# Kernel optimization log

Measured on AMD Instinct MI355X. Metric: run time of the kernel, lower is better.

The kernel has to match this reference:

```python
import jax, jax.numpy as jnp
import numpy as np

BLOCK = 16  # NVFP4 block size (one fp8e4m3 scale per 16 elements)
FP4_LEVELS = jnp.array([0.0, 0.5, 1.0, 1.5, 2.0, 3.0, 4.0, 6.0], dtype=jnp.float32)  # e2m1 magnitudes
FP4_MIDS = jnp.array([0.25, 0.75, 1.25, 1.75, 2.5, 3.5, 5.0], dtype=jnp.float32)     # round-to-nearest midpoints
FP8_MIN = 2.0 ** -9   # smallest positive fp8e4m3 subnormal (guards div-by-zero after scale cast)
FP8_MAX = 448.0


def fp8_e4m3_round(x):
    """Emulate casting positive float32 values to fp8 e4m3 (3 mantissa bits)."""
    e = jnp.clip(jnp.floor(jnp.log2(jnp.maximum(x, 1e-30))), -6.0, 8.0)  # -6 = min normal exponent
    step = jnp.exp2(e - 3.0)
    return jnp.clip(jnp.round(x / step) * step, 0.0, FP8_MAX)


def fp4_e2m1_quant(x):
    """Round-to-nearest onto the signed fp4 e2m1 grid {0,±0.5,±1,±1.5,±2,±3,±4,±6}."""
    idx = jnp.sum(jnp.abs(x)[..., None] > FP4_MIDS, axis=-1)
    return jnp.sign(x) * FP4_LEVELS[idx]


def quantize_activations(x2):
    """x2: [M, K] -> (fp4 values [M, K//16, 16], fp8 block scales [M, K//16])."""
    M, K = x2.shape
    xb = x2.reshape(M, K // BLOCK, BLOCK)
    amax = jnp.max(jnp.abs(xb), axis=-1)                      # per-16-block absmax
    s = jnp.maximum(fp8_e4m3_round(jnp.maximum(amax / 6.0, 1e-12)), FP8_MIN)
    q = fp4_e2m1_quant(xb / s[..., None])
    return q, s


def setup_inputs() -> dict:
    key = jax.random.key(0)
    k1, k2, k3 = jax.random.split(key, 3)
    in_f, out_f, tokens = 4096, 16384, 4096
    x = jax.random.normal(k1, (1, tokens, in_f), dtype=jnp.float32)
    # Build NVFP4 weights: quantize a random bf16-like weight per 16-element block.
    w = jax.random.normal(k2, (out_f, in_f), dtype=jnp.float32) * 0.02
    wb = w.reshape(out_f, in_f // BLOCK, BLOCK)
    weight_scale = jnp.maximum(fp8_e4m3_round(jnp.maximum(jnp.max(jnp.abs(wb), axis=-1) / 6.0, 1e-12)), FP8_MIN)
    weight_q = fp4_e2m1_quant(wb / weight_scale[..., None]).reshape(out_f, in_f)
    bias = jax.random.normal(k3, (out_f,), dtype=jnp.float32) * 0.01
    return {"x": x, "weight_q": weight_q, "weight_scale": weight_scale, "bias": bias}


def reference(x, weight_q, weight_scale, bias):
    orig_shape = x.shape
    K = orig_shape[-1]
    x2 = x.reshape(-1, K)                                     # [M, K]
    qa, sa = quantize_activations(x2)                          # fp4 values + fp8 block scales
    x_deq = (qa * sa[..., None]).reshape(x2.shape)             # dequantized activations
    N = weight_q.shape[0]
    w_deq = (weight_q.reshape(N, K // BLOCK, BLOCK) * weight_scale[..., None]).reshape(N, K)
    out = x2.dtype.type(0) + x_deq @ w_deq.T + bias[None, :]   # scaled_mm equivalent + bias
    return out.reshape(*orig_shape[:-1], N)
```

## Files before the change

### kernel.cpp

```cpp
#include <hip/hip_runtime.h>
#include <hip/hip_bf16.h>
#include <stdint.h>

typedef __attribute__((ext_vector_type(4))) float  f32x4;
typedef __attribute__((ext_vector_type(8))) short  bf16x8;
typedef __attribute__((ext_vector_type(8))) unsigned short u16x8;

#define MFMA16(d, x, y) d = __builtin_amdgcn_mfma_f32_16x16x32_bf16(x, y, d, 0, 0, 0)

static __device__ inline unsigned short f2bf(float f) {
    union { float f; unsigned u; } a; a.f = f;
    unsigned u = a.u;
    unsigned lsb = (u >> 16) & 1u;
    u += 0x7fffu + lsb;
    return (unsigned short)(u >> 16);
}

static __device__ inline float fp8_e4m3_round(float x) {
    union { float f; unsigned u; } a; a.f = x;
    int e = (int)((a.u >> 23) & 255u) - 127;
    e = e < -6 ? -6 : (e > 8 ? 8 : e);
    union { unsigned u; float f; } stp, inv;
    stp.u = (unsigned)(e - 3 + 127) << 23;
    inv.u = (unsigned)(3 - e + 127) << 23;
    float r = rintf(x * inv.f) * stp.f;
    return fminf(r, 448.0f);
}

static __device__ inline float fp4_level(float a) {
    return a > 2.5f ? (a > 3.5f ? (a > 5.0f ? 6.0f : 4.0f) : 3.0f)
                    : (a > 1.25f ? (a > 1.75f ? 2.0f : 1.5f)
                                 : (a > 0.75f ? 1.0f : (a > 0.25f ? 0.5f : 0.0f)));
}

__global__ void quant_x_kernel(const float* __restrict__ x, unsigned short* __restrict__ xd, int nblk) {
    int i = blockIdx.x * blockDim.x + threadIdx.x;
    if (i >= nblk) return;
    const float4* p = (const float4*)(x + (size_t)i * 16);
    float4 v0 = p[0], v1 = p[1], v2 = p[2], v3 = p[3];
    float vals[16] = { v0.x,v0.y,v0.z,v0.w, v1.x,v1.y,v1.z,v1.w,
                       v2.x,v2.y,v2.z,v2.w, v3.x,v3.y,v3.z,v3.w };
    float amax = 0.0f;
#pragma unroll
    for (int j = 0; j < 16; ++j) amax = fmaxf(amax, fabsf(vals[j]));
    float s0 = fmaxf(amax / 6.0f, 1e-12f);
    float s  = fmaxf(fp8_e4m3_round(s0), 1.0f / 512.0f);
    u16x8 o0, o1;
#pragma unroll
    for (int j = 0; j < 16; ++j) {
        float v = vals[j] / s;
        float lev = fp4_level(fabsf(v));
        float q = copysignf(lev, v);
        unsigned short b = f2bf(q * s);
        if (j < 8) o0[j] = b; else o1[j - 8] = b;
    }
    u16x8* dst = (u16x8*)(xd + (size_t)i * 16);
    dst[0] = o0; dst[1] = o1;
}

__global__ void deq_w_kernel(const float* __restrict__ wq, const float* __restrict__ wsc,
                             unsigned short* __restrict__ wd, int nblk) {
    int i = blockIdx.x * blockDim.x + threadIdx.x;
    if (i >= nblk) return;
    float s = wsc[i];
    const float4* p = (const float4*)(wq + (size_t)i * 16);
    float4 v0 = p[0], v1 = p[1], v2 = p[2], v3 = p[3];
    float vals[16] = { v0.x,v0.y,v0.z,v0.w, v1.x,v1.y,v1.z,v1.w,
                       v2.x,v2.y,v2.z,v2.w, v3.x,v3.y,v3.z,v3.w };
    u16x8 o0, o1;
#pragma unroll
    for (int j = 0; j < 16; ++j) {
        unsigned short b = f2bf(vals[j] * s);
        if (j < 8) o0[j] = b; else o1[j - 8] = b;
    }
    u16x8* dst = (u16x8*)(wd + (size_t)i * 16);
    dst[0] = o0; dst[1] = o1;
}

static __device__ __forceinline__ void stage_half(const unsigned short* g0, const unsigned short* g1,
                                                  size_t koff, char* d0) {
    __builtin_amdgcn_global_load_lds((const __attribute__((address_space(1))) void*)(g0 + koff),
                                     (__attribute__((address_space(3))) void*)d0, 16, 0, 0);
    __builtin_amdgcn_global_load_lds((const __attribute__((address_space(1))) void*)(g1 + koff),
                                     (__attribute__((address_space(3))) void*)(d0 + 1024), 16, 0, 0);
}

__global__ __launch_bounds__(512, 2)
void gemm_kernel(const unsigned short* __restrict__ A, const unsigned short* __restrict__ Bw,
                 const float* __restrict__ bias, float* __restrict__ C,
                 int M, int N, int K) {
    extern __shared__ char lds[];
    const int tid  = threadIdx.x;
    const int lane = tid & 63;
    const int wid  = tid >> 6;
    const int wr   = wid >> 2;
    const int wc   = wid & 3;

    const int NXB = N >> 8, NYB = M >> 8;
    int bid = blockIdx.x;
    int bx, by;
    if (NXB == 64 && NYB == 16) {
        int xcd = bid & 7, c = bid >> 3;
        bx = xcd * 8 + (c & 7);
        by = c >> 3;
    } else { bx = bid % NXB; by = bid / NXB; }

    const int NT = K >> 6;

    int w0 = (lane & 15) * 64 + ((lane >> 4) << 4);
    const int lane_off = w0 ^ (((w0 >> 9) & 1) << 5);
    const int u   = (lane * 16) ^ (lane & 32);
    const int r_l = u >> 6;
    const int c_l = (u & 63) >> 1;

    const unsigned short* gA0 = A  + (size_t)(by * 256 + wid * 32 + r_l) * K + c_l;
    const unsigned short* gA1 = gA0 + (size_t)16 * K;
    const unsigned short* gB0 = Bw + (size_t)(bx * 256 + wid * 32 + r_l) * K + c_l;
    const unsigned short* gB1 = gB0 + (size_t)16 * K;
    char* ldsA_w = lds + wid * 2048 + lane * 16;
    char* ldsB_w = lds + 65536 + wid * 2048 + lane * 16;

    f32x4 acc[8][4];
#pragma unroll
    for (int m = 0; m < 8; ++m)
#pragma unroll
        for (int n = 0; n < 4; ++n)
#pragma unroll
            for (int j = 0; j < 4; ++j) acc[m][n][j] = 0.0f;

    stage_half(gA0, gA1, 0,   ldsA_w);
    stage_half(gB0, gB1, 0,   ldsB_w);
    stage_half(gA0, gA1, 32,  ldsA_w + 16384);
    stage_half(gB0, gB1, 32,  ldsB_w + 16384);
    stage_half(gA0, gA1, 64,  ldsA_w + 32768);
    stage_half(gB0, gB1, 64,  ldsB_w + 32768);
    stage_half(gA0, gA1, 96,  ldsA_w + 32768 + 16384);
    asm volatile("s_waitcnt vmcnt(6)" ::: "memory");
    __builtin_amdgcn_s_barrier();

    bf16x8 a[8], bq[4];

    for (int t = 0; t <= NT - 3; ++t) {
        const int b = t & 1;
        const char* pA = lds + b * 32768 + wr * 8192 + lane_off;
        const char* pB = lds + 65536 + b * 32768 + wc * 4096 + lane_off;
        char* dA2 = ldsA_w + b * 32768;
        char* dB1 = ldsB_w + ((t + 1) & 1) * 32768;
        char* dB2 = ldsB_w + b * 32768;
        const size_t k1off = (size_t)(t + 1) * 64;
        const size_t k2off = (size_t)(t + 2) * 64;

        asm volatile("s_waitcnt vmcnt(6)" ::: "memory");
#pragma unroll
        for (int mf = 0; mf < 8; ++mf) a[mf] = *(const bf16x8*)(pA + mf * 1024);
        bq[0] = *(const bf16x8*)(pB);
        bq[1] = *(const bf16x8*)(pB + 1024);
        stage_half(gB0, gB1, k1off + 32, dB1 + 16384);
        __builtin_amdgcn_s_barrier();
        asm volatile("s_waitcnt lgkmcnt(0)" ::: "memory");
        __builtin_amdgcn_s_setprio(1);
#pragma unroll
        for (int mf = 0; mf < 8; ++mf) { MFMA16(acc[mf][0], a[mf], bq[0]); MFMA16(acc[mf][1], a[mf], bq[1]); }
        __builtin_amdgcn_s_setprio(0);
        __builtin_amdgcn_s_barrier();

        bq[2] = *(const bf16x8*)(pB + 2048);
        bq[3] = *(const bf16x8*)(pB + 3072);
        stage_half(gA0, gA1, k2off, dA2);
        __builtin_amdgcn_s_barrier();
        asm volatile("s_waitcnt lgkmcnt(0)" ::: "memory");
        __builtin_amdgcn_s_setprio(1);
#pragma unroll
        for (int mf = 0; mf < 8; ++mf) { MFMA16(acc[mf][2], a[mf], bq[2]); MFMA16(acc[mf][3], a[mf], bq[3]); }
        __builtin_amdgcn_s_setprio(0);
        __builtin_amdgcn_s_barrier();

        asm volatile("s_waitcnt vmcnt(6)" ::: "memory");
#pragma unroll
        for (int mf = 0; mf < 8; ++mf) a[mf] = *(const bf16x8*)(pA + 16384 + mf * 1024);
        bq[0] = *(const bf16x8*)(pB + 16384);
        bq[1] = *(const bf16x8*)(pB + 16384 + 1024);
        stage_half(gB0, gB1, k2off, dB2);
        __builtin_amdgcn_s_barrier();
        asm volatile("s_waitcnt lgkmcnt(0)" ::: "memory");
        __builtin_amdgcn_s_setprio(1);
#pragma unroll
        for (int mf = 0; mf < 8; ++mf) { MFMA16(acc[mf][0], a[mf], bq[0]); MFMA16(acc[mf][1], a[mf], bq[1]); }
        __builtin_amdgcn_s_setprio(0);
        __builtin_amdgcn_s_barrier();

        bq[2] = *(const bf16x8*)(pB + 16384 + 2048);
        bq[3] = *(const bf16x8*)(pB + 16384 + 3072);
        stage_half(gA0, gA1, k2off + 32, dA2 + 16384);
        __builtin_amdgcn_s_barrier();
        asm volatile("s_waitcnt lgkmcnt(0)" ::: "memory");
        __builtin_amdgcn_s_setprio(1);
#pragma unroll
        for (int mf = 0; mf < 8; ++mf) { MFMA16(acc[mf][2], a[mf], bq[2]); MFMA16(acc[mf][3], a[mf], bq[3]); }
        __builtin_amdgcn_s_setprio(0);
        __builtin_amdgcn_s_barrier();
    }

    {
        char* dBl = ldsB_w + ((NT - 1) & 1) * 32768;
        stage_half(gB0, gB1, (size_t)(NT - 1) * 64 + 32, dBl + 16384);
    }
    asm volatile("s_waitcnt vmcnt(0)" ::: "memory");
    __builtin_amdgcn_s_barrier();

#pragma unroll 1
    for (int tt = NT - 2; tt < NT; ++tt) {
        const int b = tt & 1;
        const char* pA = lds + b * 32768 + wr * 8192 + lane_off;
        const char* pB = lds + 65536 + b * 32768 + wc * 4096 + lane_off;
#pragma unroll
        for (int s = 0; s < 2; ++s) {
            bf16x8 a2[8], b2[4];
#pragma unroll
            for (int mf = 0; mf < 8; ++mf) a2[mf] = *(const bf16x8*)(pA + s * 16384 + mf * 1024);
#pragma unroll
            for (int nf = 0; nf < 4; ++nf) b2[nf] = *(const bf16x8*)(pB + s * 16384 + nf * 1024);
#pragma unroll
            for (int mf = 0; mf < 8; ++mf)
#pragma unroll
                for (int nf = 0; nf < 4; ++nf) MFMA16(acc[mf][nf], a2[mf], b2[nf]);
        }
    }

    const int row0 = by * 256 + wr * 128;
    const int col0 = bx * 256 + wc * 64;
#pragma unroll
    for (int nf = 0; nf < 4; ++nf) {
        int col = col0 + nf * 16 + (lane & 15);
        float bv = bias[col];
#pragma unroll
        for (int mf = 0; mf < 8; ++mf) {
#pragma unroll
            for (int j = 0; j < 4; ++j) {
                int row = row0 + mf * 16 + ((lane >> 4) << 2) + j;
                C[(size_t)row * N + col] = acc[mf][nf][j] + bv;
            }
        }
    }
}

extern "C" void kernel_launch(void* const* d_in, const int* in_sizes, int n_in,
                              void* d_out, int out_size, void* d_ws, size_t ws_size,
                              hipStream_t stream) {
    const float* x    = (const float*)d_in[0];
    const float* wq   = (const float*)d_in[1];
    const float* wsc  = (const float*)d_in[2];
    const float* bias = (const float*)d_in[3];
    float* out = (float*)d_out;

    const long N = in_sizes[3];
    const long K = (long)in_sizes[1] / N;
    const long M = (long)in_sizes[0] / K;

    size_t need = ((size_t)(M * K) + (size_t)(N * K)) * sizeof(unsigned short);
    if (ws_size < need) return;

    unsigned short* xd = (unsigned short*)d_ws;
    unsigned short* wd = xd + (size_t)M * K;

    {
        int nblk = (int)(M * K / 16);
        quant_x_kernel<<<(nblk + 255) / 256, 256, 0, stream>>>(x, xd, nblk);
    }
    {
        int nblk = (int)(N * K / 16);
        deq_w_kernel<<<(nblk + 255) / 256, 256, 0, stream>>>(wq, wsc, wd, nblk);
    }
    {
        hipFuncSetAttribute((const void*)gemm_kernel,
                            hipFuncAttributeMaxDynamicSharedMemorySize, 131072);
        int nwg = (int)((M / 256) * (N / 256));
        gemm_kernel<<<dim3(nwg), dim3(512), 131072, stream>>>(xd, wd, bias, out,
                                                              (int)M, (int)N, (int)K);
    }
}
```

Before: 539.9 us.

## Restructure GEMM main loop into register double-buffered M-half quadrants

The main loop now splits each K-step into M-half by full-N MFMA blocks instead of N-half by full-M blocks. A and B fragments are preloaded into separate register sets so LDS reads for the next quadrant or K-step are issued before the current MFMAs. Partial lgkmcnt waits and sched_barriers are meant to overlap LDS latency with matrix math. The cost is higher VGPR pressure from the extra fragment buffers, and the global-to-LDS staging order is changed, which risks data races if the barrier placement is wrong.

```diff
diff --git a/kernel.cpp b/kernel.cpp
--- a/kernel.cpp
+++ b/kernel.cpp
@@ -138,65 +138,85 @@
     asm volatile("s_waitcnt vmcnt(6)" ::: "memory");
     __builtin_amdgcn_s_barrier();
 
-    bf16x8 a[8], bq[4];
+    bf16x8 aK0a[4], aK0b[4], aK1a[4], aK1b[4], bK0[4], bK1[4];
+
+    {
+        const char* pA = lds + wr * 8192 + lane_off;
+        const char* pB = lds + 65536 + wc * 4096 + lane_off;
+#pragma unroll
+        for (int i = 0; i < 4; ++i) aK0a[i] = *(const bf16x8*)(pA + i * 1024);
+#pragma unroll
+        for (int i = 0; i < 4; ++i) bK0[i]  = *(const bf16x8*)(pB + i * 1024);
+    }
 
     for (int t = 0; t <= NT - 3; ++t) {
-        const int b = t & 1;
-        const char* pA = lds + b * 32768 + wr * 8192 + lane_off;
-        const char* pB = lds + 65536 + b * 32768 + wc * 4096 + lane_off;
+        const int b  = t & 1;
+        const int b1 = (t + 1) & 1;
+        const char* pA  = lds + b * 32768 + wr * 8192 + lane_off;
+        const char* pB  = lds + 65536 + b * 32768 + wc * 4096 + lane_off;
+        const char* pA1 = lds + b1 * 32768 + wr * 8192 + lane_off;
+        const char* pB1 = lds + 65536 + b1 * 32768 + wc * 4096 + lane_off;
         char* dA2 = ldsA_w + b * 32768;
-        char* dB1 = ldsB_w + ((t + 1) & 1) * 32768;
+        char* dB1 = ldsB_w + b1 * 32768;
         char* dB2 = ldsB_w + b * 32768;
         const size_t k1off = (size_t)(t + 1) * 64;
         const size_t k2off = (size_t)(t + 2) * 64;
 
+#pragma unroll
+        for (int i = 0; i < 4; ++i) aK0b[i] = *(const bf16x8*)(pA + (4 + i) * 1024);
+        stage_half(gB0, gB1, k1off + 32, dB1 + 16384);
+        __builtin_amdgcn_s_barrier();
+        __builtin_amdgcn_s_setprio(1);
+#pragma unroll
+        for (int m = 0; m < 4; ++m)
+#pragma unroll
+            for (int n = 0; n < 4; ++n) MFMA16(acc[m][n], aK0a[m], bK0[n]);
+        __builtin_amdgcn_s_setprio(0);
+        __builtin_amdgcn_s_barrier();
+
         asm volatile("s_waitcnt vmcnt(6)" ::: "memory");
 #pragma unroll
-        for (int mf = 0; mf < 8; ++mf) a[mf] = *(const bf16x8*)(pA + mf * 1024);
-        bq[0] = *(const bf16x8*)(pB);
-        bq[1] = *(const bf16x8*)(pB + 1024);
-        stage_half(gB0, gB1, k1off + 32, dB1 + 16384);
-        __builtin_amdgcn_s_barrier();
-        asm volatile("s_waitcnt lgkmcnt(0)" ::: "memory");
+        for (int i = 0; i < 4; ++i) aK1a[i] = *(const bf16x8*)(pA + 16384 + i * 1024);
+#pragma unroll
+        for (int i = 0; i < 4; ++i) bK1[i]  = *(const bf16x8*)(pB + 16384 + i * 1024);
+        __builtin_amdgcn_s_barrier();
+        asm volatile("s_waitcnt lgkmcnt(8)" ::: "memory");
+        __builtin_amdgcn_sched_barrier(0);
+        stage_half(gA0, gA1, k2off, dA2);
         __builtin_amdgcn_s_setprio(1);
 #pragma unroll
-        for (int mf = 0; mf < 8; ++mf) { MFMA16(acc[mf][0], a[mf], bq[0]); MFMA16(acc[mf][1], a[mf], bq[1]); }
+        for (int m = 0; m < 4; ++m)
+#pragma unroll
+            for (int n = 0; n < 4; ++n) MFMA16(acc[4 + m][n], aK0b[m], bK0[n]);
         __builtin_amdgcn_s_setprio(0);
         __builtin_amdgcn_s_barrier();
 
-        bq[2] = *(const bf16x8*)(pB + 2048);
-        bq[3] = *(const bf16x8*)(pB + 3072);
-        stage_half(gA0, gA1, k2off, dA2);
-        __builtin_amdgcn_s_barrier();
-        asm volatile("s_waitcnt lgkmcnt(0)" ::: "memory");
+#pragma unroll
+        for (int i = 0; i < 4; ++i) aK1b[i] = *(const bf16x8*)(pA + 16384 + (4 + i) * 1024);
+        stage_half(gB0, gB1, k2off, dB2);
+        __builtin_amdgcn_s_barrier();
         __builtin_amdgcn_s_setprio(1);
 #pragma unroll
-        for (int mf = 0; mf < 8; ++mf) { MFMA16(acc[mf][2], a[mf], bq[2]); MFMA16(acc[mf][3], a[mf], bq[3]); }
+        for (int m = 0; m < 4; ++m)
+#pragma unroll
+            for (int n = 0; n < 4; ++n) MFMA16(acc[m][n], aK1a[m], bK1[n]);
         __builtin_amdgcn_s_setprio(0);
         __builtin_amdgcn_s_barrier();
 
         asm volatile("s_waitcnt vmcnt(6)" ::: "memory");
 #pragma unroll
-        for (int mf = 0; mf < 8; ++mf) a[mf] = *(const bf16x8*)(pA + 16384 + mf * 1024);
-        bq[0] = *(const bf16x8*)(pB + 16384);
-        bq[1] = *(const bf16x8*)(pB + 16384 + 1024);
-        stage_half(gB0, gB1, k2off, dB2);
-        __builtin_amdgcn_s_barrier();
-        asm volatile("s_waitcnt lgkmcnt(0)" ::: "memory");
+        for (int i = 0; i < 4; ++i) aK0a[i] = *(const bf16x8*)(pA1 + i * 1024);
+#pragma unroll
+        for (int i = 0; i < 4; ++i) bK0[i]  = *(const bf16x8*)(pB1 + i * 1024);
+        __builtin_amdgcn_s_barrier();
+        asm volatile("s_waitcnt lgkmcnt(8)" ::: "memory");
+        __builtin_amdgcn_sched_barrier(0);
+        stage_half(gA0, gA1, k2off + 32, dA2 + 16384);
         __builtin_amdgcn_s_setprio(1);
 #pragma unroll
-        for (int mf = 0; mf < 8; ++mf) { MFMA16(acc[mf][0], a[mf], bq[0]); MFMA16(acc[mf][1], a[mf], bq[1]); }
-        __builtin_amdgcn_s_setprio(0);
-        __builtin_amdgcn_s_barrier();
-
-        bq[2] = *(const bf16x8*)(pB + 16384 + 2048);
-        bq[3] = *(const bf16x8*)(pB + 16384 + 3072);
-        stage_half(gA0, gA1, k2off + 32, dA2 + 16384);
-        __builtin_amdgcn_s_barrier();
-        asm volatile("s_waitcnt lgkmcnt(0)" ::: "memory");
-        __builtin_amdgcn_s_setprio(1);
-#pragma unroll
-        for (int mf = 0; mf < 8; ++mf) { MFMA16(acc[mf][2], a[mf], bq[2]); MFMA16(acc[mf][3], a[mf], bq[3]); }
+        for (int m = 0; m < 4; ++m)
+#pragma unroll
+            for (int n = 0; n < 4; ++n) MFMA16(acc[4 + m][n], aK1b[m], bK1[n]);
         __builtin_amdgcn_s_setprio(0);
         __builtin_amdgcn_s_barrier();
     }
```

Measured after the change: 559.4 us. 3.6% more time.

## Load B fragments directly from global into registers, stage only A in LDS

Applied to the files above, without the earlier changes.

The GEMM no longer stages the weight (B) tile through LDS. Each wave loads its B fragments straight from global memory into registers, double-buffered across iterations, while A is still staged with global_load_lds. The main loop is unrolled by two with a macro body, and LDS use drops from 128KB to 64KB. This removes LDS traffic and bank pressure for B, but each B element is now fetched from global once per wave row instead of once per workgroup (duplicated across the two wr waves), and it adds register pressure.

```diff
diff --git a/kernel.cpp b/kernel.cpp
--- a/kernel.cpp
+++ b/kernel.cpp
@@ -85,6 +85,60 @@
                                      (__attribute__((address_space(3))) void*)(d0 + 1024), 16, 0, 0);
 }
 
+#define LOADB4(dst, koff) {                                             \
+    dst[0] = *(const bf16x8*)(gBr + (size_t)(koff));                    \
+    dst[1] = *(const bf16x8*)(gBr + bstride + (size_t)(koff));          \
+    dst[2] = *(const bf16x8*)(gBr + 2 * bstride + (size_t)(koff));      \
+    dst[3] = *(const bf16x8*)(gBr + 3 * bstride + (size_t)(koff)); }
+
+#define MFMA_HALF(AV, BV, n0) {                                         \
+    _Pragma("unroll")                                                   \
+    for (int mf = 0; mf < 8; ++mf) {                                    \
+        MFMA16(acc[mf][n0], AV[mf], BV[n0]);                            \
+        MFMA16(acc[mf][n0 + 1], AV[mf], BV[n0 + 1]);                    \
+    } }
+
+#define BODY(T, BUFC, BUFN, K0C, K1C, K0N) {                                      \
+    const size_t t64 = (size_t)(T) * 64;                                          \
+                                                                          \
+    LOADB4(K1C, t64 + 32);                                                        \
+    __builtin_amdgcn_s_barrier();                                                 \
+    asm volatile("s_waitcnt lgkmcnt(0)" ::: "memory");                            \
+    __builtin_amdgcn_s_setprio(1);                                                \
+    MFMA_HALF(a, K0C, 0);                                                         \
+    __builtin_amdgcn_s_setprio(0);                                                \
+    __builtin_amdgcn_s_barrier();                                                 \
+                                                                          \
+    stage_half(gA0, gA1, t64 + 128, ldsA_w + (BUFC) * 32768);                     \
+    { const char* pc = lds + (BUFC) * 32768 + wr * 8192 + lane_off + 16384;       \
+      _Pragma("unroll")                                                           \
+      for (int i = 0; i < 8; ++i) a2[i] = *(const bf16x8*)(pc + i * 1024); }      \
+    asm volatile("s_waitcnt vmcnt(12)" ::: "memory");                             \
+    __builtin_amdgcn_s_barrier();                                                 \
+    __builtin_amdgcn_s_setprio(1);                                                \
+    MFMA_HALF(a, K0C, 2);                                                         \
+    __builtin_amdgcn_s_setprio(0);                                                \
+    __builtin_amdgcn_s_barrier();                                                 \
+                                                                          \
+    LOADB4(K0N, t64 + 64);                                                        \
+    __builtin_amdgcn_s_barrier();                                                 \
+    asm volatile("s_waitcnt lgkmcnt(0)" ::: "memory");                            \
+    __builtin_amdgcn_s_setprio(1);                                                \
+    MFMA_HALF(a2, K1C, 0);                                                        \
+    __builtin_amdgcn_s_setprio(0);                                                \
+    __builtin_amdgcn_s_barrier();                                                 \
+                                                                          \
+    stage_half(gA0, gA1, t64 + 160, ldsA_w + (BUFC) * 32768 + 16384);             \
+    { const char* pn = lds + (BUFN) * 32768 + wr * 8192 + lane_off;               \
+      _Pragma("unroll")                                                           \
+      for (int i = 0; i < 8; ++i) a[i] = *(const bf16x8*)(pn + i * 1024); }       \
+    asm volatile("s_waitcnt vmcnt(12)" ::: "memory");                             \
+    __builtin_amdgcn_s_barrier();                                                 \
+    __builtin_amdgcn_s_setprio(1);                                                \
+    MFMA_HALF(a2, K1C, 2);                                                        \
+    __builtin_amdgcn_s_setprio(0);                                                \
+    __builtin_amdgcn_s_barrier(); }
+
 __global__ __launch_bounds__(512, 2)
 void gemm_kernel(const unsigned short* __restrict__ A, const unsigned short* __restrict__ Bw,
                  const float* __restrict__ bias, float* __restrict__ C,
@@ -113,12 +167,13 @@
     const int r_l = u >> 6;
     const int c_l = (u & 63) >> 1;
 
-    const unsigned short* gA0 = A  + (size_t)(by * 256 + wid * 32 + r_l) * K + c_l;
+    const unsigned short* gA0 = A + (size_t)(by * 256 + wid * 32 + r_l) * K + c_l;
     const unsigned short* gA1 = gA0 + (size_t)16 * K;
-    const unsigned short* gB0 = Bw + (size_t)(bx * 256 + wid * 32 + r_l) * K + c_l;
-    const unsigned short* gB1 = gB0 + (size_t)16 * K;
     char* ldsA_w = lds + wid * 2048 + lane * 16;
-    char* ldsB_w = lds + 65536 + wid * 2048 + lane * 16;
+
+    const size_t bstride = (size_t)16 * K;
+    const unsigned short* gBr = Bw + (size_t)(bx * 256 + wc * 64 + (lane & 15)) * K
+                                   + ((lane >> 4) << 3);
 
     f32x4 acc[8][4];
 #pragma unroll
@@ -128,104 +183,52 @@
 #pragma unroll
             for (int j = 0; j < 4; ++j) acc[m][n][j] = 0.0f;
 
+    bf16x8 a[8], a2[8];
+    bf16x8 b0x[4], b1x[4], b0y[4], b1y[4];
+
     stage_half(gA0, gA1, 0,   ldsA_w);
-    stage_half(gB0, gB1, 0,   ldsB_w);
     stage_half(gA0, gA1, 32,  ldsA_w + 16384);
-    stage_half(gB0, gB1, 32,  ldsB_w + 16384);
     stage_half(gA0, gA1, 64,  ldsA_w + 32768);
-    stage_half(gB0, gB1, 64,  ldsB_w + 32768);
     stage_half(gA0, gA1, 96,  ldsA_w + 32768 + 16384);
-    asm volatile("s_waitcnt vmcnt(6)" ::: "memory");
+    LOADB4(b0x, 0);
+    asm volatile("s_waitcnt vmcnt(8)" ::: "memory");
     __builtin_amdgcn_s_barrier();
-
-    bf16x8 a[8], bq[4];
-
-    for (int t = 0; t <= NT - 3; ++t) {
-        const int b = t & 1;
-        const char* pA = lds + b * 32768 + wr * 8192 + lane_off;
-        const char* pB = lds + 65536 + b * 32768 + wc * 4096 + lane_off;
-        char* dA2 = ldsA_w + b * 32768;
-        char* dB1 = ldsB_w + ((t + 1) & 1) * 32768;
-        char* dB2 = ldsB_w + b * 32768;
-        const size_t k1off = (size_t)(t + 1) * 64;
-        const size_t k2off = (size_t)(t + 2) * 64;
-
-        asm volatile("s_waitcnt vmcnt(6)" ::: "memory");
-#pragma unroll
-        for (int mf = 0; mf < 8; ++mf) a[mf] = *(const bf16x8*)(pA + mf * 1024);
-        bq[0] = *(const bf16x8*)(pB);
-        bq[1] = *(const bf16x8*)(pB + 1024);
-        stage_half(gB0, gB1, k1off + 32, dB1 + 16384);
-        __builtin_amdgcn_s_barrier();
-        asm volatile("s_waitcnt lgkmcnt(0)" ::: "memory");
-        __builtin_amdgcn_s_setprio(1);
-#pragma unroll
-        for (int mf = 0; mf < 8; ++mf) { MFMA16(acc[mf][0], a[mf], bq[0]); MFMA16(acc[mf][1], a[mf], bq[1]); }
-        __builtin_amdgcn_s_setprio(0);
-        __builtin_amdgcn_s_barrier();
-
-        bq[2] = *(const bf16x8*)(pB + 2048);
-        bq[3] = *(const bf16x8*)(pB + 3072);
-        stage_half(gA0, gA1, k2off, dA2);
-        __builtin_amdgcn_s_barrier();
-        asm volatile("s_waitcnt lgkmcnt(0)" ::: "memory");
-        __builtin_amdgcn_s_setprio(1);
-#pragma unroll
-        for (int mf = 0; mf < 8; ++mf) { MFMA16(acc[mf][2], a[mf], bq[2]); MFMA16(acc[mf][3], a[mf], bq[3]); }
-        __builtin_amdgcn_s_setprio(0);
-        __builtin_amdgcn_s_barrier();
-
-        asm volatile("s_waitcnt vmcnt(6)" ::: "memory");
-#pragma unroll
-        for (int mf = 0; mf < 8; ++mf) a[mf] = *(const bf16x8*)(pA + 16384 + mf * 1024);
-        bq[0] = *(const bf16x8*)(pB + 16384);
-        bq[1] = *(const bf16x8*)(pB + 16384 + 1024);
-        stage_half(gB0, gB1, k2off, dB2);
-        __builtin_amdgcn_s_barrier();
-        asm volatile("s_waitcnt lgkmcnt(0)" ::: "memory");
-        __builtin_amdgcn_s_setprio(1);
-#pragma unroll
-        for (int mf = 0; mf < 8; ++mf) { MFMA16(acc[mf][0], a[mf], bq[0]); MFMA16(acc[mf][1], a[mf], bq[1]); }
-        __builtin_amdgcn_s_setprio(0);
-        __builtin_amdgcn_s_barrier();
-
-        bq[2] = *(const bf16x8*)(pB + 16384 + 2048);
-        bq[3] = *(const bf16x8*)(pB + 16384 + 3072);
-        stage_half(gA0, gA1, k2off + 32, dA2 + 16384);
-        __builtin_amdgcn_s_barrier();
-        asm volatile("s_waitcnt lgkmcnt(0)" ::: "memory");
-        __builtin_amdgcn_s_setprio(1);
-#pragma unroll
-        for (int mf = 0; mf < 8; ++mf) { MFMA16(acc[mf][2], a[mf], bq[2]); MFMA16(acc[mf][3], a[mf], bq[3]); }
-        __builtin_amdgcn_s_setprio(0);
-        __builtin_amdgcn_s_barrier();
-    }
-
-    {
-        char* dBl = ldsB_w + ((NT - 1) & 1) * 32768;
-        stage_half(gB0, gB1, (size_t)(NT - 1) * 64 + 32, dBl + 16384);
-    }
+    {
+        const char* p0 = lds + wr * 8192 + lane_off;
+#pragma unroll
+        for (int i = 0; i < 8; ++i) a[i] = *(const bf16x8*)(p0 + i * 1024);
+    }
+
+    for (int t = 0; t <= NT - 4; t += 2) {
+        BODY(t,     0, 1, b0x, b1x, b0y);
+        BODY(t + 1, 1, 0, b0y, b1y, b0x);
+    }
+
+    LOADB4(b1x, (size_t)(NT - 2) * 64 + 32);
+    LOADB4(b0y, (size_t)(NT - 1) * 64);
+    LOADB4(b1y, (size_t)(NT - 1) * 64 + 32);
     asm volatile("s_waitcnt vmcnt(0)" ::: "memory");
     __builtin_amdgcn_s_barrier();
-
-#pragma unroll 1
-    for (int tt = NT - 2; tt < NT; ++tt) {
-        const int b = tt & 1;
-        const char* pA = lds + b * 32768 + wr * 8192 + lane_off;
-        const char* pB = lds + 65536 + b * 32768 + wc * 4096 + lane_off;
-#pragma unroll
-        for (int s = 0; s < 2; ++s) {
-            bf16x8 a2[8], b2[4];
-#pragma unroll
-            for (int mf = 0; mf < 8; ++mf) a2[mf] = *(const bf16x8*)(pA + s * 16384 + mf * 1024);
-#pragma unroll
-            for (int nf = 0; nf < 4; ++nf) b2[nf] = *(const bf16x8*)(pB + s * 16384 + nf * 1024);
-#pragma unroll
-            for (int mf = 0; mf < 8; ++mf)
-#pragma unroll
-                for (int nf = 0; nf < 4; ++nf) MFMA16(acc[mf][nf], a2[mf], b2[nf]);
-        }
-    }
+    asm volatile("s_waitcnt lgkmcnt(0)" ::: "memory");
+    MFMA_HALF(a, b0x, 0); MFMA_HALF(a, b0x, 2);
+    {
+        const char* pc = lds + wr * 8192 + lane_off + 16384;
+#pragma unroll
+        for (int i = 0; i < 8; ++i) a2[i] = *(const bf16x8*)(pc + i * 1024);
+    }
+    MFMA_HALF(a2, b1x, 0); MFMA_HALF(a2, b1x, 2);
+    {
+        const char* pn = lds + 32768 + wr * 8192 + lane_off;
+#pragma unroll
+        for (int i = 0; i < 8; ++i) a[i] = *(const bf16x8*)(pn + i * 1024);
+    }
+    MFMA_HALF(a, b0y, 0); MFMA_HALF(a, b0y, 2);
+    {
+        const char* pn2 = lds + 32768 + wr * 8192 + lane_off + 16384;
+#pragma unroll
+        for (int i = 0; i < 8; ++i) a2[i] = *(const bf16x8*)(pn2 + i * 1024);
+    }
+    MFMA_HALF(a2, b1y, 0); MFMA_HALF(a2, b1y, 2);
 
     const int row0 = by * 256 + wr * 128;
     const int col0 = bx * 256 + wc * 64;
@@ -273,9 +276,9 @@
     }
     {
         hipFuncSetAttribute((const void*)gemm_kernel,
-                            hipFuncAttributeMaxDynamicSharedMemorySize, 131072);
+                            hipFuncAttributeMaxDynamicSharedMemorySize, 65536);
         int nwg = (int)((M / 256) * (N / 256));
-        gemm_kernel<<<dim3(nwg), dim3(512), 131072, stream>>>(xd, wd, bias, out,
-                                                              (int)M, (int)N, (int)K);
-    }
-}
+        gemm_kernel<<<dim3(nwg), dim3(512), 65536, stream>>>(xd, wd, bias, out,
+                                                             (int)M, (int)N, (int)K);
+    }
+}
```

Measured after the change: 1.039 ms. 92.4% more time.

## Register double-buffer LDS fragments and overlap reads with full MFMA phases

Applied to the files above, without the earlier changes.

Restructures the GEMM main loop so that each phase holds two register sets of A/B fragments. The next half-tile is read from LDS while the 32 MFMAs of the current half run, with one barrier per phase instead of four. Global-to-LDS staging is reorganised so both A and B halves load together, and the prologue and epilogue are adjusted to match. The aim is to hide LDS read latency and barrier overhead, at the cost of higher register pressure and less margin on the LDS write-after-read ordering.

```diff
diff --git a/kernel.cpp b/kernel.cpp
--- a/kernel.cpp
+++ b/kernel.cpp
@@ -85,6 +85,40 @@
                                      (__attribute__((address_space(3))) void*)(d0 + 1024), 16, 0, 0);
 }
 
+#define MFMA_ALL(AV, BV) {                                              \
+    _Pragma("unroll")                                                   \
+    for (int mf = 0; mf < 8; ++mf) {                                    \
+        _Pragma("unroll")                                               \
+        for (int nf = 0; nf < 4; ++nf) MFMA16(acc[mf][nf], AV[mf], BV[nf]); } }
+
+#define READ12(AV, BV, OFF) {                                           \
+    const char* _pa = lds + (OFF) + wr * 8192 + lane_off;               \
+    const char* _pb = lds + 65536 + (OFF) + wc * 4096 + lane_off;       \
+    _Pragma("unroll")                                                   \
+    for (int i = 0; i < 8; ++i) AV[i] = *(const bf16x8*)(_pa + i * 1024); \
+    _Pragma("unroll")                                                   \
+    for (int i = 0; i < 4; ++i) BV[i] = *(const bf16x8*)(_pb + i * 1024); }
+
+#define PH1(T, B) {                                                     \
+    asm volatile("s_waitcnt vmcnt(4)" ::: "memory");                    \
+    __builtin_amdgcn_s_barrier();                                       \
+    __builtin_amdgcn_s_setprio(1);                                      \
+    READ12(a2, b2, (B) * 32768 + 16384);                                \
+    stage_half(gA0, gA1, (size_t)((T) + 1) * 64 + 32, ldsA_w + (1 - (B)) * 32768 + 16384); \
+    stage_half(gB0, gB1, (size_t)((T) + 1) * 64 + 32, ldsB_w + (1 - (B)) * 32768 + 16384); \
+    MFMA_ALL(a1, b1);                                                   \
+    __builtin_amdgcn_s_setprio(0); }
+
+#define PH2(T, B) {                                                     \
+    asm volatile("s_waitcnt vmcnt(4)" ::: "memory");                    \
+    __builtin_amdgcn_s_barrier();                                       \
+    __builtin_amdgcn_s_setprio(1);                                      \
+    READ12(a1, b1, (1 - (B)) * 32768);                                  \
+    stage_half(gA0, gA1, (size_t)((T) + 2) * 64, ldsA_w + (B) * 32768); \
+    stage_half(gB0, gB1, (size_t)((T) + 2) * 64, ldsB_w + (B) * 32768); \
+    MFMA_ALL(a2, b2);                                                   \
+    __builtin_amdgcn_s_setprio(0); }
+
 __global__ __launch_bounds__(512, 2)
 void gemm_kernel(const unsigned short* __restrict__ A, const unsigned short* __restrict__ Bw,
                  const float* __restrict__ bias, float* __restrict__ C,
@@ -128,103 +162,36 @@
 #pragma unroll
             for (int j = 0; j < 4; ++j) acc[m][n][j] = 0.0f;
 
-    stage_half(gA0, gA1, 0,   ldsA_w);
-    stage_half(gB0, gB1, 0,   ldsB_w);
-    stage_half(gA0, gA1, 32,  ldsA_w + 16384);
-    stage_half(gB0, gB1, 32,  ldsB_w + 16384);
-    stage_half(gA0, gA1, 64,  ldsA_w + 32768);
-    stage_half(gB0, gB1, 64,  ldsB_w + 32768);
-    stage_half(gA0, gA1, 96,  ldsA_w + 32768 + 16384);
-    asm volatile("s_waitcnt vmcnt(6)" ::: "memory");
+    bf16x8 a1[8], a2[8], b1[4], b2[4];
+
+    stage_half(gA0, gA1, 0,  ldsA_w);
+    stage_half(gB0, gB1, 0,  ldsB_w);
+    stage_half(gA0, gA1, 32, ldsA_w + 16384);
+    stage_half(gB0, gB1, 32, ldsB_w + 16384);
+    stage_half(gA0, gA1, 64, ldsA_w + 32768);
+    stage_half(gB0, gB1, 64, ldsB_w + 32768);
+    asm volatile("s_waitcnt vmcnt(8)" ::: "memory");
     __builtin_amdgcn_s_barrier();
-
-    bf16x8 a[8], bq[4];
-
-    for (int t = 0; t <= NT - 3; ++t) {
-        const int b = t & 1;
-        const char* pA = lds + b * 32768 + wr * 8192 + lane_off;
-        const char* pB = lds + 65536 + b * 32768 + wc * 4096 + lane_off;
-        char* dA2 = ldsA_w + b * 32768;
-        char* dB1 = ldsB_w + ((t + 1) & 1) * 32768;
-        char* dB2 = ldsB_w + b * 32768;
-        const size_t k1off = (size_t)(t + 1) * 64;
-        const size_t k2off = (size_t)(t + 2) * 64;
-
-        asm volatile("s_waitcnt vmcnt(6)" ::: "memory");
-#pragma unroll
-        for (int mf = 0; mf < 8; ++mf) a[mf] = *(const bf16x8*)(pA + mf * 1024);
-        bq[0] = *(const bf16x8*)(pB);
-        bq[1] = *(const bf16x8*)(pB + 1024);
-        stage_half(gB0, gB1, k1off + 32, dB1 + 16384);
+    READ12(a1, b1, 0);
+
+    for (int t = 0; t <= NT - 4; t += 2) {
+        PH1(t, 0);  PH2(t, 0);
+        PH1(t + 1, 1);  PH2(t + 1, 1);
+    }
+
+    PH1(NT - 2, 0);
+    {
+        asm volatile("s_waitcnt vmcnt(4)" ::: "memory");
         __builtin_amdgcn_s_barrier();
-        asm volatile("s_waitcnt lgkmcnt(0)" ::: "memory");
-        __builtin_amdgcn_s_setprio(1);
-#pragma unroll
-        for (int mf = 0; mf < 8; ++mf) { MFMA16(acc[mf][0], a[mf], bq[0]); MFMA16(acc[mf][1], a[mf], bq[1]); }
-        __builtin_amdgcn_s_setprio(0);
+        READ12(a1, b1, 32768);
+        MFMA_ALL(a2, b2);
+    }
+    {
+        asm volatile("s_waitcnt vmcnt(0)" ::: "memory");
         __builtin_amdgcn_s_barrier();
-
-        bq[2] = *(const bf16x8*)(pB + 2048);
-        bq[3] = *(const bf16x8*)(pB + 3072);
-        stage_half(gA0, gA1, k2off, dA2);
-        __builtin_amdgcn_s_barrier();
-        asm volatile("s_waitcnt lgkmcnt(0)" ::: "memory");
-        __builtin_amdgcn_s_setprio(1);
-#pragma unroll
-        for (int mf = 0; mf < 8; ++mf) { MFMA16(acc[mf][2], a[mf], bq[2]); MFMA16(acc[mf][3], a[mf], bq[3]); }
-        __builtin_amdgcn_s_setprio(0);
-        __builtin_amdgcn_s_barrier();
-
-        asm volatile("s_waitcnt vmcnt(6)" ::: "memory");
-#pragma unroll
-        for (int mf = 0; mf < 8; ++mf) a[mf] = *(const bf16x8*)(pA + 16384 + mf * 1024);
-        bq[0] = *(const bf16x8*)(pB + 16384);
-        bq[1] = *(const bf16x8*)(pB + 16384 + 1024);
-        stage_half(gB0, gB1, k2off, dB2);
-        __builtin_amdgcn_s_barrier();
-        asm volatile("s_waitcnt lgkmcnt(0)" ::: "memory");
-        __builtin_amdgcn_s_setprio(1);
-#pragma unroll
-        for (int mf = 0; mf < 8; ++mf) { MFMA16(acc[mf][0], a[mf], bq[0]); MFMA16(acc[mf][1], a[mf], bq[1]); }
-        __builtin_amdgcn_s_setprio(0);
-        __builtin_amdgcn_s_barrier();
-
-        bq[2] = *(const bf16x8*)(pB + 16384 + 2048);
-        bq[3] = *(const bf16x8*)(pB + 16384 + 3072);
-        stage_half(gA0, gA1, k2off + 32, dA2 + 16384);
-        __builtin_amdgcn_s_barrier();
-        asm volatile("s_waitcnt lgkmcnt(0)" ::: "memory");
-        __builtin_amdgcn_s_setprio(1);
-#pragma unroll
-        for (int mf = 0; mf < 8; ++mf) { MFMA16(acc[mf][2], a[mf], bq[2]); MFMA16(acc[mf][3], a[mf], bq[3]); }
-        __builtin_amdgcn_s_setprio(0);
-        __builtin_amdgcn_s_barrier();
-    }
-
-    {
-        char* dBl = ldsB_w + ((NT - 1) & 1) * 32768;
-        stage_half(gB0, gB1, (size_t)(NT - 1) * 64 + 32, dBl + 16384);
-    }
-    asm volatile("s_waitcnt vmcnt(0)" ::: "memory");
-    __builtin_amdgcn_s_barrier();
-
-#pragma unroll 1
-    for (int tt = NT - 2; tt < NT; ++tt) {
-        const int b = tt & 1;
-        const char* pA = lds + b * 32768 + wr * 8192 + lane_off;
-        const char* pB = lds + 65536 + b * 32768 + wc * 4096 + lane_off;
-#pragma unroll
-        for (int s = 0; s < 2; ++s) {
-            bf16x8 a2[8], b2[4];
-#pragma unroll
-            for (int mf = 0; mf < 8; ++mf) a2[mf] = *(const bf16x8*)(pA + s * 16384 + mf * 1024);
-#pragma unroll
-            for (int nf = 0; nf < 4; ++nf) b2[nf] = *(const bf16x8*)(pB + s * 16384 + nf * 1024);
-#pragma unroll
-            for (int mf = 0; mf < 8; ++mf)
-#pragma unroll
-                for (int nf = 0; nf < 4; ++nf) MFMA16(acc[mf][nf], a2[mf], b2[nf]);
-        }
+        READ12(a2, b2, 32768 + 16384);
+        MFMA_ALL(a1, b1);
+        MFMA_ALL(a2, b2);
     }
 
     const int row0 = by * 256 + wr * 128;
```

Result: no change. 545.4 us (+1.0%).
